# Performance work log

Measured on AMD Instinct MI355X. Metric: run time of the kernel, lower is better.

Reference implementation:

```python
import jax, jax.numpy as jnp
import numpy as np

K = 20
EPS = 1e-5
NEG_SLOPE = 0.2


def _bn(x, gamma, beta, axes):
    # batch-norm in training mode (batch statistics), per-channel on last axis
    mean = jnp.mean(x, axis=axes, keepdims=True)
    var = jnp.var(x, axis=axes, keepdims=True)
    return gamma * (x - mean) * jax.lax.rsqrt(var + EPS) + beta


def _lrelu(x):
    return jnp.where(x >= 0, x, NEG_SLOPE * x)


def setup_inputs() -> dict:
    key = jax.random.key(0)
    ks = jax.random.split(key, 8)
    B, C, N = 8, 6, 4096

    def w(k_, shape):
        fan_in = shape[-1]
        return jax.random.normal(k_, shape, jnp.float32) / np.sqrt(fan_in)

    return {
        "x": jax.random.normal(ks[0], (B, C, N), jnp.float32),
        "conv1_w": w(ks[1], (64, 12)),
        "bn1_g": jnp.ones((64,), jnp.float32), "bn1_b": jnp.zeros((64,), jnp.float32),
        "conv2_w": w(ks[2], (128, 64)),
        "bn2_g": jnp.ones((128,), jnp.float32), "bn2_b": jnp.zeros((128,), jnp.float32),
        "conv3_w": w(ks[3], (1024, 128)),
        "bn3_g": jnp.ones((1024,), jnp.float32), "bn3_b": jnp.zeros((1024,), jnp.float32),
        "fc1_w": w(ks[4], (512, 1024)),
        "bn4_g": jnp.ones((512,), jnp.float32), "bn4_b": jnp.zeros((512,), jnp.float32),
        "fc2_w": w(ks[5], (256, 512)),
        "bn5_g": jnp.ones((256,), jnp.float32), "bn5_b": jnp.zeros((256,), jnp.float32),
        "fc3_w": w(ks[6], (9, 256)), "fc3_b": jnp.zeros((9,), jnp.float32),
        "fc4_w": w(ks[7], (3, 256)), "fc4_b": jnp.zeros((3,), jnp.float32),
    }


def _get_graph_feature(x, k):
    # x: [B, C, N] -> [B, N, k, 2C]
    B, C, N = x.shape
    xt = jnp.transpose(x, (0, 2, 1))                      # [B, N, C]
    xx = jnp.sum(xt * xt, axis=-1)                        # [B, N]
    inner = jnp.einsum('bnc,bmc->bnm', xt, xt)            # [B, N, N]
    pd = 2.0 * inner - xx[:, :, None] - xx[:, None, :]    # -||xi-xj||^2
    _, idx = jax.lax.top_k(pd, k)                         # [B, N, k]
    nbr = xt[jnp.arange(B)[:, None, None], idx]           # [B, N, k, C]
    center = jnp.broadcast_to(xt[:, :, None, :], nbr.shape)
    return jnp.concatenate([nbr - center, center], axis=-1)  # [B, N, k, 2C]


def reference(x, conv1_w, bn1_g, bn1_b, conv2_w, bn2_g, bn2_b,
              conv3_w, bn3_g, bn3_b, fc1_w, bn4_g, bn4_b,
              fc2_w, bn5_g, bn5_b, fc3_w, fc3_b, fc4_w, fc4_b):
    B = x.shape[0]
    feat = _get_graph_feature(x, K)                            # [B, N, k, 12]
    h = _lrelu(_bn(jnp.einsum('bnkc,oc->bnko', feat, conv1_w), bn1_g, bn1_b, (0, 1, 2)))
    h = _lrelu(_bn(jnp.einsum('bnkc,oc->bnko', h, conv2_w), bn2_g, bn2_b, (0, 1, 2)))
    h = jnp.max(h, axis=2)                                     # [B, N, 128] max over k
    h = _lrelu(_bn(jnp.einsum('bnc,oc->bno', h, conv3_w), bn3_g, bn3_b, (0, 1)))
    g = jnp.max(h, axis=1)                                     # [B, 1024] max over points
    g = _lrelu(_bn(g @ fc1_w.T, bn4_g, bn4_b, (0,)))           # [B, 512]
    g = _lrelu(_bn(g @ fc2_w.T, bn5_g, bn5_b, (0,)))           # [B, 256]
    bias = (g @ fc4_w.T + fc4_b)[:, None, :]                   # [B, 1, 3]
    matrix = jnp.eye(3, dtype=x.dtype) + (g @ fc3_w.T + fc3_b).reshape(B, 3, 3)
    xyz = jnp.transpose(x[:, :3, :], (0, 2, 1))                # [B, N, 3]
    out = jnp.einsum('bnc,bcd->bnd', xyz, matrix) + bias       # [B, N, 3]
    return jnp.transpose(out, (0, 2, 1))                       # [B, 3, N]
```

## Files before the change

kernel.cpp:

```cpp
#include <hip/hip_runtime.h>
#include <math.h>
#include <stddef.h>


static constexpr float EPS_ = 1e-5f;

__global__ __launch_bounds__(256) void k_prep(const float* __restrict__ x,
                                              float* __restrict__ xtp)
{
    int i = blockIdx.x*256 + threadIdx.x;
    int b = i >> 12, n = i & 4095;
    const float* xb = x + (size_t)b*6*4096 + n;
    float v0 = xb[0], v1 = xb[4096], v2 = xb[2*4096];
    float v3 = xb[3*4096], v4 = xb[4*4096], v5 = xb[5*4096];
    float xx = v0*v0 + v1*v1 + v2*v2 + v3*v3 + v4*v4 + v5*v5;
    float4* o = (float4*)(xtp + (size_t)i*8);
    o[0] = make_float4(v0, v1, v2, v3);
    o[1] = make_float4(v4, v5, xx, 0.f);
}

__device__ __forceinline__ float pd_calc(const float4 a0, const float4 a1,
                                         const float4 q0, const float4 q1)
{
    float dot = a0.x*q0.x;
    dot = fmaf(a0.y, q0.y, dot);
    dot = fmaf(a0.z, q0.z, dot);
    dot = fmaf(a0.w, q0.w, dot);
    dot = fmaf(a1.x, q1.x, dot);
    dot = fmaf(a1.y, q1.y, dot);
    return fmaf(2.f, dot, -a1.z - q1.z);
}

#define TK_CAP 384
__global__ __launch_bounds__(256) void k_topk(const float* __restrict__ xtp,
                                              int* __restrict__ idxout)
{
    __shared__ float maxs[4][256];
    __shared__ float candv[4][TK_CAP];
    __shared__ int   candi[4][TK_CAP];
    __shared__ float Ts[4];
    __shared__ unsigned ccnt[4];

    const int t = threadIdx.x;
    const int rowbase = blockIdx.x << 2;
    const int b = rowbase >> 12;
    const float* xb = xtp + ((size_t)b << 15);

    float4 c0[4], c1[4];
    #pragma unroll
    for (int c = 0; c < 4; c++){
        const float4* p = (const float4*)(xtp + (size_t)(rowbase + c)*8);
        c0[c] = p[0]; c1[c] = p[1];
    }

    float mx[4] = {-INFINITY, -INFINITY, -INFINITY, -INFINITY};
    for (int i = 0; i < 16; i++){
        const float4* p = (const float4*)(xb + (size_t)((i << 8) | t)*8);
        float4 q0 = p[0], q1 = p[1];
        #pragma unroll
        for (int c = 0; c < 4; c++)
            mx[c] = fmaxf(mx[c], pd_calc(c0[c], c1[c], q0, q1));
    }
    #pragma unroll
    for (int c = 0; c < 4; c++) maxs[c][t] = mx[c];
    if (t < 4) ccnt[t] = 0u;
    __syncthreads();

    const int w = t >> 6, lane = t & 63;
    {
        float v[4];
        #pragma unroll
        for (int j = 0; j < 4; j++) v[j] = maxs[w][(j << 6) | lane];
        float gv = -INFINITY;
        for (int r = 0; r < 20; r++){
            float bv = fmaxf(fmaxf(v[0], v[1]), fmaxf(v[2], v[3]));
            gv = bv;
            #pragma unroll
            for (int s = 1; s < 64; s <<= 1) gv = fmaxf(gv, __shfl_xor(gv, s));
            if (bv == gv){
                if      (v[0] == gv) v[0] = -INFINITY;
                else if (v[1] == gv) v[1] = -INFINITY;
                else if (v[2] == gv) v[2] = -INFINITY;
                else                 v[3] = -INFINITY;
            }
        }
        if (lane == 0) Ts[w] = gv;
    }
    __syncthreads();

    #pragma unroll
    for (int c = 0; c < 4; c++){
        if (mx[c] >= Ts[c]){
            float Tc = Ts[c];
            for (int i = 0; i < 16; i++){
                int m = (i << 8) | t;
                const float4* p = (const float4*)(xb + (size_t)m*8);
                float4 q0 = p[0], q1 = p[1];
                float pd = pd_calc(c0[c], c1[c], q0, q1);
                if (pd >= Tc){
                    unsigned pos = atomicAdd(&ccnt[c], 1u);
                    if (pos < TK_CAP){ candv[c][pos] = pd; candi[c][pos] = m; }
                }
            }
        }
    }
    __syncthreads();

    {
        int n = (int)min(ccnt[w], (unsigned)TK_CAP);
        float v[6]; int id[6];
        #pragma unroll
        for (int j = 0; j < 6; j++){
            int p = (j << 6) | lane;
            bool ok = p < n;
            v[j]  = ok ? candv[w][p] : -INFINITY;
            id[j] = ok ? candi[w][p] : 0x7fffffff;
        }
        int* out = idxout + (size_t)(rowbase + w)*20;
        for (int r = 0; r < 20; r++){
            float bv = -INFINITY; int bi = 0x7fffffff, bj = 0;
            #pragma unroll
            for (int j = 0; j < 6; j++){
                bool better = (v[j] > bv) || (v[j] == bv && id[j] < bi);
                if (better){ bv = v[j]; bi = id[j]; bj = j; }
            }
            float gv = bv; int gi = bi;
            #pragma unroll
            for (int s = 1; s < 64; s <<= 1){
                float ov = __shfl_xor(gv, s); int oi = __shfl_xor(gi, s);
                if (ov > gv || (ov == gv && oi < gi)){ gv = ov; gi = oi; }
            }
            if (lane == 0) out[r] = (gi == 0x7fffffff) ? 0 : gi;
            if (bi == gi){ v[bj] = -INFINITY; id[bj] = 0x7fffffff; }
        }
    }
}

__global__ __launch_bounds__(256) void k_bn1stats(const float* __restrict__ xtp,
                                                  const int* __restrict__ idxb,
                                                  const float* __restrict__ w1,
                                                  float* __restrict__ bn1sum,
                                                  float* __restrict__ bn1sq)
{
    __shared__ float fT[320*12];
    __shared__ float red[2][4][64];
    const int t = threadIdx.x;
    const int rowbase = blockIdx.x << 4;
    const int b = rowbase >> 12;

    for (int s = t; s < 320; s += 256){
        int r = s / 20, k = s % 20;
        int grow = rowbase + r;
        int m = idxb[(size_t)grow*20 + k];
        const float4* pn = (const float4*)(xtp + (size_t)((b << 12) | m)*8);
        const float4* pc = (const float4*)(xtp + (size_t)grow*8);
        float4 n0 = pn[0], n1 = pn[1], c0 = pc[0], c1 = pc[1];
        float* f = fT + s*12;
        ((float4*)f)[0] = make_float4(n0.x-c0.x, n0.y-c0.y, n0.z-c0.z, n0.w-c0.w);
        ((float4*)f)[1] = make_float4(n1.x-c1.x, n1.y-c1.y, c0.x, c0.y);
        ((float4*)f)[2] = make_float4(c0.z, c0.w, c1.x, c1.y);
    }
    __syncthreads();
    const int o = t & 63, grp = t >> 6;
    float w[12];
    #pragma unroll
    for (int c = 0; c < 12; c++) w[c] = w1[o*12 + c];
    float sm = 0.f, sq = 0.f;
    for (int s = grp*80; s < grp*80 + 80; s++){
        const float* f = fT + s*12;
        float4 f0 = *(const float4*)(f);
        float4 fa = *(const float4*)(f + 4);
        float4 fb = *(const float4*)(f + 8);
        float h = w[0]*f0.x + w[1]*f0.y + w[2]*f0.z + w[3]*f0.w
                + w[4]*fa.x + w[5]*fa.y + w[6]*fa.z + w[7]*fa.w
                + w[8]*fb.x + w[9]*fb.y + w[10]*fb.z + w[11]*fb.w;
        sm += h; sq = fmaf(h, h, sq);
    }
    red[0][grp][o] = sm; red[1][grp][o] = sq;
    __syncthreads();
    if (t < 64){
        float a = red[0][0][t] + red[0][1][t] + red[0][2][t] + red[0][3][t];
        float c2 = red[1][0][t] + red[1][1][t] + red[1][2][t] + red[1][3][t];
        atomicAdd(bn1sum + t, a);
        atomicAdd(bn1sq + t, c2);
    }
}

__global__ void k_bnfin(const float* __restrict__ sum, const float* __restrict__ sq,
                        const float* __restrict__ gamma, const float* __restrict__ beta,
                        float* __restrict__ st, int C, float invN)
{
    int o = threadIdx.x;
    if (o < C){
        float mean = sum[o]*invN;
        float var  = sq[o]*invN - mean*mean;
        float s = gamma[o]/sqrtf(var + EPS_);
        st[o] = s;
        st[C + o] = beta[o] - mean*s;
    }
}

__global__ __launch_bounds__(256) void k_conv12(
    const float* __restrict__ xtp, const int* __restrict__ idxb,
    const float* __restrict__ w1, const float* __restrict__ w2,
    const float* __restrict__ bn1st,
    float* __restrict__ h2max, float* __restrict__ bn2sum, float* __restrict__ bn2sq)
{
    __shared__ float fT[4*20*12];
    __shared__ float f1s[4*20*64];
    __shared__ float w2t[64*132];
    __shared__ float w1s[64*13];
    const int t = threadIdx.x;
    const int rowbase = blockIdx.x << 2;
    const int b = rowbase >> 12;

    for (int e = t; e < 64*12; e += 256) w1s[(e/12)*13 + (e%12)] = w1[e];
    for (int e = t; e < 128*64; e += 256) w2t[(e & 63)*132 + (e >> 6)] = w2[e];
    if (t < 80){
        int r = t / 20, k = t % 20;
        int grow = rowbase + r;
        int m = idxb[(size_t)grow*20 + k];
        const float4* pn = (const float4*)(xtp + (size_t)((b << 12) | m)*8);
        const float4* pc = (const float4*)(xtp + (size_t)grow*8);
        float4 n0 = pn[0], n1 = pn[1], c0 = pc[0], c1 = pc[1];
        float* f = fT + (r*20 + k)*12;
        ((float4*)f)[0] = make_float4(n0.x-c0.x, n0.y-c0.y, n0.z-c0.z, n0.w-c0.w);
        ((float4*)f)[1] = make_float4(n1.x-c1.x, n1.y-c1.y, c0.x, c0.y);
        ((float4*)f)[2] = make_float4(c0.z, c0.w, c1.x, c1.y);
    }
    __syncthreads();
    {
        const int j = t & 63;
        const float s1 = bn1st[j], t1 = bn1st[64 + j];
        float wr[12];
        #pragma unroll
        for (int c = 0; c < 12; c++) wr[c] = w1s[j*13 + c];
        for (int vid = t; vid < 4*20*64; vid += 256){
            const float* f = fT + (vid >> 6)*12;
            float4 f0 = *(const float4*)(f);
            float4 fa = *(const float4*)(f + 4);
            float4 fb = *(const float4*)(f + 8);
            float acc = wr[0]*f0.x + wr[1]*f0.y + wr[2]*f0.z + wr[3]*f0.w
                      + wr[4]*fa.x + wr[5]*fa.y + wr[6]*fa.z + wr[7]*fa.w
                      + wr[8]*fb.x + wr[9]*fb.y + wr[10]*fb.z + wr[11]*fb.w;
            float v = fmaf(s1, acc, t1);
            f1s[vid] = fmaxf(v, 0.2f*v);
        }
    }
    __syncthreads();
    const int oq = t & 31, kslot = t >> 5;
    const int o0 = oq << 2;
    float mx[4][4], sm[4][4], sq[4][4];
    #pragma unroll
    for (int r = 0; r < 4; r++)
        #pragma unroll
        for (int i = 0; i < 4; i++){ mx[r][i] = -INFINITY; sm[r][i] = 0.f; sq[r][i] = 0.f; }
    for (int k = kslot; k < 20; k += 8){
        float h[4][4];
        #pragma unroll
        for (int r = 0; r < 4; r++){ h[r][0]=0.f; h[r][1]=0.f; h[r][2]=0.f; h[r][3]=0.f; }
        for (int j = 0; j < 64; j += 4){
            float wv[4][4];
            #pragma unroll
            for (int jj = 0; jj < 4; jj++)
                *(float4*)wv[jj] = *(const float4*)&w2t[(j + jj)*132 + o0];
            #pragma unroll
            for (int r = 0; r < 4; r++){
                float fv[4];
                *(float4*)fv = *(const float4*)&f1s[((r*20 + k) << 6) + j];
                #pragma unroll
                for (int jj = 0; jj < 4; jj++)
                    #pragma unroll
                    for (int oi = 0; oi < 4; oi++)
                        h[r][oi] = fmaf(fv[jj], wv[jj][oi], h[r][oi]);
            }
        }
        #pragma unroll
        for (int r = 0; r < 4; r++)
            #pragma unroll
            for (int oi = 0; oi < 4; oi++){
                mx[r][oi] = fmaxf(mx[r][oi], h[r][oi]);
                sm[r][oi] += h[r][oi];
                sq[r][oi] = fmaf(h[r][oi], h[r][oi], sq[r][oi]);
            }
    }
    __syncthreads();
    #pragma unroll
    for (int r = 0; r < 4; r++)
        *(float4*)&f1s[((kslot << 2) + r)*128 + o0] = make_float4(mx[r][0], mx[r][1], mx[r][2], mx[r][3]);
    __syncthreads();
    for (int it = t; it < 512; it += 256){
        int r = it >> 7, o = it & 127;
        float m = f1s[r*128 + o];
        #pragma unroll
        for (int ks = 1; ks < 8; ks++) m = fmaxf(m, f1s[((ks << 2) + r)*128 + o]);
        h2max[(size_t)(rowbase + r)*128 + o] = m;
    }
    __syncthreads();
    #pragma unroll
    for (int r = 0; r < 4; r++)
        *(float4*)&f1s[((kslot << 2) + r)*128 + o0] = make_float4(sm[r][0], sm[r][1], sm[r][2], sm[r][3]);
    __syncthreads();
    if (t < 128){
        float s = 0.f;
        #pragma unroll
        for (int i = 0; i < 32; i++) s += f1s[i*128 + t];
        atomicAdd(bn2sum + t, s);
    }
    __syncthreads();
    #pragma unroll
    for (int r = 0; r < 4; r++)
        *(float4*)&f1s[((kslot << 2) + r)*128 + o0] = make_float4(sq[r][0], sq[r][1], sq[r][2], sq[r][3]);
    __syncthreads();
    if (t < 128){
        float s = 0.f;
        #pragma unroll
        for (int i = 0; i < 32; i++) s += f1s[i*128 + t];
        atomicAdd(bn2sq + t, s);
    }
}

__global__ __launch_bounds__(256) void k_conv3(const float* __restrict__ h2max,
    const float* __restrict__ bn2st, const float* __restrict__ w3,
    float* __restrict__ bn3sum, float* __restrict__ bn3sq, unsigned int* __restrict__ gkey)
{
    __shared__ float f2[32*132];
    __shared__ float w3t[128*68];
    const int t = threadIdx.x;
    const int rt = blockIdx.x >> 4;
    const int ot = blockIdx.x & 15;
    const int rowbase = rt << 5;
    const int obase = ot << 6;
    const int b = rowbase >> 12;

    for (int e = t; e < 32*128; e += 256){
        int r = e >> 7, c = e & 127;
        float v = h2max[(size_t)(rowbase + r)*128 + c];
        float u = fmaf(bn2st[c], v, bn2st[128 + c]);
        f2[r*132 + c] = fmaxf(u, 0.2f*u);
    }
    for (int e = t; e < 64*128; e += 256){
        int ol = e >> 7, j = e & 127;
        w3t[j*68 + ol] = w3[(size_t)(obase + ol)*128 + j];
    }
    __syncthreads();
    const int oq = t & 15, rg = t >> 4;
    const int o0 = oq << 2, r0 = rg << 1;
    float h0[4] = {0.f,0.f,0.f,0.f}, h1[4] = {0.f,0.f,0.f,0.f};
    for (int j = 0; j < 128; j += 4){
        float wv[4][4];
        #pragma unroll
        for (int jj = 0; jj < 4; jj++)
            *(float4*)wv[jj] = *(const float4*)&w3t[(j + jj)*68 + o0];
        float fa[4], fb[4];
        *(float4*)fa = *(const float4*)&f2[r0*132 + j];
        *(float4*)fb = *(const float4*)&f2[(r0 + 1)*132 + j];
        #pragma unroll
        for (int jj = 0; jj < 4; jj++)
            #pragma unroll
            for (int oi = 0; oi < 4; oi++){
                h0[oi] = fmaf(fa[jj], wv[jj][oi], h0[oi]);
                h1[oi] = fmaf(fb[jj], wv[jj][oi], h1[oi]);
            }
    }
    __syncthreads();
    float* scratch = f2;
    *(float4*)&scratch[(rg << 6) + o0] =
        make_float4(h0[0]+h1[0], h0[1]+h1[1], h0[2]+h1[2], h0[3]+h1[3]);
    __syncthreads();
    if (t < 64){
        float s = 0.f;
        #pragma unroll
        for (int g2 = 0; g2 < 16; g2++) s += scratch[(g2 << 6) + t];
        atomicAdd(bn3sum + obase + t, s);
    }
    __syncthreads();
    *(float4*)&scratch[(rg << 6) + o0] =
        make_float4(h0[0]*h0[0]+h1[0]*h1[0], h0[1]*h0[1]+h1[1]*h1[1],
                    h0[2]*h0[2]+h1[2]*h1[2], h0[3]*h0[3]+h1[3]*h1[3]);
    __syncthreads();
    if (t < 64){
        float s = 0.f;
        #pragma unroll
        for (int g2 = 0; g2 < 16; g2++) s += scratch[(g2 << 6) + t];
        atomicAdd(bn3sq + obase + t, s);
    }
    __syncthreads();
    *(float4*)&scratch[(rg << 6) + o0] =
        make_float4(fmaxf(h0[0],h1[0]), fmaxf(h0[1],h1[1]),
                    fmaxf(h0[2],h1[2]), fmaxf(h0[3],h1[3]));
    __syncthreads();
    if (t < 64){
        float m = scratch[t];
        #pragma unroll
        for (int g2 = 1; g2 < 16; g2++) m = fmaxf(m, scratch[(g2 << 6) + t]);
        unsigned u = __float_as_uint(m);
        unsigned key = (u & 0x80000000u) ? ~u : (u | 0x80000000u);
        atomicMax(gkey + (b << 10) + obase + t, key);
    }
}

__global__ void k_bn3g(const float* __restrict__ sum, const float* __restrict__ sq,
                       const unsigned int* __restrict__ gkey,
                       const float* __restrict__ gamma, const float* __restrict__ beta,
                       float* __restrict__ g)
{
    int o = blockIdx.x*256 + threadIdx.x;
    if (o < 1024){
        float mean = sum[o]*(1.f/32768.f);
        float var  = sq[o]*(1.f/32768.f) - mean*mean;
        float s = gamma[o]/sqrtf(var + EPS_);
        float tt = beta[o] - mean*s;
        for (int b = 0; b < 8; b++){
            unsigned k = gkey[(b << 10) + o];
            unsigned u = (k & 0x80000000u) ? (k & 0x7fffffffu) : ~k;
            float v = __uint_as_float(u);
            float xv = fmaf(s, v, tt);
            g[(b << 10) + o] = fmaxf(xv, 0.2f*xv);
        }
    }
}

__global__ __launch_bounds__(256) void k_fc(const float* __restrict__ in,
                                            const float* __restrict__ w,
                                            float* __restrict__ out, int Kdim, int Odim)
{
    int wid = (blockIdx.x*256 + threadIdx.x) >> 6;
    int lane = threadIdx.x & 63;
    int nout = 8*Odim;
    if (wid >= nout) return;
    int b = wid / Odim, o = wid - b*Odim;
    const float* gi = in + (size_t)b*Kdim;
    const float* wr = w + (size_t)o*Kdim;
    float acc = 0.f;
    for (int c = lane; c < Kdim; c += 64) acc = fmaf(gi[c], wr[c], acc);
    #pragma unroll
    for (int s = 32; s > 0; s >>= 1) acc += __shfl_xor(acc, s);
    if (lane == 0) out[(size_t)b*Odim + o] = acc;
}

__global__ void k_bnb(const float* __restrict__ h, const float* __restrict__ gamma,
                      const float* __restrict__ beta, float* __restrict__ g, int C)
{
    int o = blockIdx.x*256 + threadIdx.x;
    if (o < C){
        float s = 0.f, q = 0.f;
        for (int b = 0; b < 8; b++){ float v = h[(size_t)b*C + o]; s += v; q = fmaf(v, v, q); }
        float mean = s*0.125f;
        float var  = q*0.125f - mean*mean;
        float sc = gamma[o]/sqrtf(var + EPS_);
        float tt = beta[o] - mean*sc;
        for (int b = 0; b < 8; b++){
            float xv = fmaf(sc, h[(size_t)b*C + o], tt);
            g[(size_t)b*C + o] = fmaxf(xv, 0.2f*xv);
        }
    }
}

__global__ void k_head(const float* __restrict__ g5,
                       const float* __restrict__ fc3w, const float* __restrict__ fc3b,
                       const float* __restrict__ fc4w, const float* __restrict__ fc4b,
                       float* __restrict__ mat, float* __restrict__ bias3)
{
    int t = threadIdx.x;
    if (t < 96){
        int b = t / 12, j = t % 12;
        const float* gi = g5 + b*256;
        if (j < 9){
            const float* w = fc3w + j*256;
            float a = fc3b[j];
            for (int c = 0; c < 256; c++) a = fmaf(gi[c], w[c], a);
            if (j == 0 || j == 4 || j == 8) a += 1.f;
            mat[b*9 + j] = a;
        } else {
            int d = j - 9;
            const float* w = fc4w + d*256;
            float a = fc4b[d];
            for (int c = 0; c < 256; c++) a = fmaf(gi[c], w[c], a);
            bias3[b*3 + d] = a;
        }
    }
}

__global__ __launch_bounds__(256) void k_out(const float* __restrict__ x,
                                             const float* __restrict__ mat,
                                             const float* __restrict__ bias3,
                                             float* __restrict__ out)
{
    int i = blockIdx.x*256 + threadIdx.x;
    int n = i & 4095, bd = i >> 12;
    int b = bd / 3, d = bd - b*3;
    const float* xb = x + (size_t)b*6*4096 + n;
    const float* M = mat + b*9;
    out[i] = xb[0]*M[d] + xb[4096]*M[3 + d] + xb[2*4096]*M[6 + d] + bias3[b*3 + d];
}

extern "C" void kernel_launch(void* const* d_in, const int* in_sizes, int n_in,
                              void* d_out, int out_size, void* d_ws, size_t ws_size,
                              hipStream_t stream)
{
    const float* x     = (const float*)d_in[0];
    const float* w1    = (const float*)d_in[1];
    const float* bn1g  = (const float*)d_in[2];
    const float* bn1b  = (const float*)d_in[3];
    const float* w2    = (const float*)d_in[4];
    const float* bn2g  = (const float*)d_in[5];
    const float* bn2b  = (const float*)d_in[6];
    const float* w3    = (const float*)d_in[7];
    const float* bn3gm = (const float*)d_in[8];
    const float* bn3bt = (const float*)d_in[9];
    const float* fc1w  = (const float*)d_in[10];
    const float* bn4g  = (const float*)d_in[11];
    const float* bn4b  = (const float*)d_in[12];
    const float* fc2w  = (const float*)d_in[13];
    const float* bn5g  = (const float*)d_in[14];
    const float* bn5b  = (const float*)d_in[15];
    const float* fc3w  = (const float*)d_in[16];
    const float* fc3b  = (const float*)d_in[17];
    const float* fc4w  = (const float*)d_in[18];
    const float* fc4b  = (const float*)d_in[19];
    float* out = (float*)d_out;

    char* ws = (char*)d_ws;
    float* xtp   = (float*)(ws);
    int*   idxb  = (int*)  (ws + 1048576);
    float* h2max = (float*)(ws + 3670016);
    float* zs    = (float*)(ws + 20447232);
    float* bn1sum = zs;            float* bn1sq = zs + 64;
    float* bn2sum = zs + 128;      float* bn2sq = zs + 256;
    float* bn3sum = zs + 384;      float* bn3sq = zs + 1408;
    unsigned int* gkey = (unsigned int*)(zs + 2432);
    float* tail  = (float*)(ws + 20489728);
    float* bn1st = tail;
    float* bn2st = tail + 128;
    float* g     = tail + 384;
    float* h4    = tail + 8576;
    float* g4    = tail + 12672;
    float* h5    = tail + 16768;
    float* g5    = tail + 18816;
    float* mat   = tail + 20864;
    float* bias3 = tail + 20936;

    hipMemsetAsync(zs, 0, 42496, stream);

    k_prep    <<<128,   256, 0, stream>>>(x, xtp);
    k_topk    <<<8192,  256, 0, stream>>>(xtp, idxb);
    k_bn1stats<<<2048,  256, 0, stream>>>(xtp, idxb, w1, bn1sum, bn1sq);
    k_bnfin   <<<1,     128, 0, stream>>>(bn1sum, bn1sq, bn1g, bn1b, bn1st, 64, 1.f/655360.f);
    k_conv12  <<<8192,  256, 0, stream>>>(xtp, idxb, w1, w2, bn1st, h2max, bn2sum, bn2sq);
    k_bnfin   <<<1,     128, 0, stream>>>(bn2sum, bn2sq, bn2g, bn2b, bn2st, 128, 1.f/655360.f);
    k_conv3   <<<16384, 256, 0, stream>>>(h2max, bn2st, w3, bn3sum, bn3sq, gkey);
    k_bn3g    <<<4,     256, 0, stream>>>(bn3sum, bn3sq, gkey, bn3gm, bn3bt, g);
    k_fc      <<<1024,  256, 0, stream>>>(g, fc1w, h4, 1024, 512);
    k_bnb     <<<2,     256, 0, stream>>>(h4, bn4g, bn4b, g4, 512);
    k_fc      <<<512,   256, 0, stream>>>(g4, fc2w, h5, 512, 256);
    k_bnb     <<<1,     256, 0, stream>>>(h5, bn5g, bn5b, g5, 256);
    k_head    <<<1,     128, 0, stream>>>(g5, fc3w, fc3b, fc4w, fc4b, mat, bias3);
    k_out     <<<384,   256, 0, stream>>>(x, mat, bias3, out);
}
```

Before: 808.0 us.

## Split conv12 output channels across two blocks and swizzle the feature tile in LDS

Each k_conv12 block now computes only 64 of the 128 conv2 output channels, and the grid is doubled. This shrinks the staged w2 tile and drops the separate w1 copy from shared memory, so more blocks can be resident per CU; launch bounds request 4 blocks. The conv1 feature tile in LDS gets an XOR swizzle to avoid bank conflicts on the float4 reads. The cost is that every conv1 activation is computed twice, the gather is repeated per half, and the 16 k-slots spread over 20 neighbours leave the per-thread work uneven.

```diff
diff --git a/kernel.cpp b/kernel.cpp
--- a/kernel.cpp
+++ b/kernel.cpp
@@ -200,22 +200,24 @@
     }
 }
 
-__global__ __launch_bounds__(256) void k_conv12(
+__global__ __launch_bounds__(256, 4) void k_conv12(
     const float* __restrict__ xtp, const int* __restrict__ idxb,
     const float* __restrict__ w1, const float* __restrict__ w2,
     const float* __restrict__ bn1st,
     float* __restrict__ h2max, float* __restrict__ bn2sum, float* __restrict__ bn2sq)
 {
-    __shared__ float fT[4*20*12];
-    __shared__ float f1s[4*20*64];
-    __shared__ float w2t[64*132];
-    __shared__ float w1s[64*13];
+    __shared__ float fT[80*12];
+    __shared__ float f1s[80*64];
+    __shared__ float w2t[64*65];
     const int t = threadIdx.x;
-    const int rowbase = blockIdx.x << 2;
+    const int rowbase = (blockIdx.x >> 1) << 2;
+    const int obase   = (blockIdx.x & 1) << 6;
     const int b = rowbase >> 12;
 
-    for (int e = t; e < 64*12; e += 256) w1s[(e/12)*13 + (e%12)] = w1[e];
-    for (int e = t; e < 128*64; e += 256) w2t[(e & 63)*132 + (e >> 6)] = w2[e];
+    for (int e = t; e < 64*64; e += 256){
+        int ol = e >> 6, j = e & 63;
+        w2t[j*65 + ol] = w2[(size_t)(obase + ol)*64 + j];
+    }
     if (t < 80){
         int r = t / 20, k = t % 20;
         int grow = rowbase + r;
@@ -223,7 +225,7 @@
         const float4* pn = (const float4*)(xtp + (size_t)((b << 12) | m)*8);
         const float4* pc = (const float4*)(xtp + (size_t)grow*8);
         float4 n0 = pn[0], n1 = pn[1], c0 = pc[0], c1 = pc[1];
-        float* f = fT + (r*20 + k)*12;
+        float* f = fT + t*12;
         ((float4*)f)[0] = make_float4(n0.x-c0.x, n0.y-c0.y, n0.z-c0.z, n0.w-c0.w);
         ((float4*)f)[1] = make_float4(n1.x-c1.x, n1.y-c1.y, c0.x, c0.y);
         ((float4*)f)[2] = make_float4(c0.z, c0.w, c1.x, c1.y);
@@ -234,9 +236,11 @@
         const float s1 = bn1st[j], t1 = bn1st[64 + j];
         float wr[12];
         #pragma unroll
-        for (int c = 0; c < 12; c++) wr[c] = w1s[j*13 + c];
-        for (int vid = t; vid < 4*20*64; vid += 256){
-            const float* f = fT + (vid >> 6)*12;
+        for (int cc = 0; cc < 12; cc++) wr[cc] = w1[j*12 + cc];
+        const int sw_off = (((j >> 2) ) << 2) | (j & 3);
+        for (int vid = t; vid < 80*64; vid += 256){
+            int p = vid >> 6;
+            const float* f = fT + p*12;
             float4 f0 = *(const float4*)(f);
             float4 fa = *(const float4*)(f + 4);
             float4 fb = *(const float4*)(f + 8);
@@ -244,18 +248,20 @@
                       + wr[4]*fa.x + wr[5]*fa.y + wr[6]*fa.z + wr[7]*fa.w
                       + wr[8]*fb.x + wr[9]*fb.y + wr[10]*fb.z + wr[11]*fb.w;
             float v = fmaf(s1, acc, t1);
-            f1s[vid] = fmaxf(v, 0.2f*v);
-        }
-    }
-    __syncthreads();
-    const int oq = t & 31, kslot = t >> 5;
+            v = fmaxf(v, 0.2f*v);
+            f1s[(p << 6) + (((((j >> 2) ^ (p & 3))) << 2) | (j & 3))] = v;
+        }
+        (void)sw_off;
+    }
+    __syncthreads();
+    const int oq = t & 15, ks = t >> 4;
     const int o0 = oq << 2;
     float mx[4][4], sm[4][4], sq[4][4];
     #pragma unroll
     for (int r = 0; r < 4; r++)
         #pragma unroll
         for (int i = 0; i < 4; i++){ mx[r][i] = -INFINITY; sm[r][i] = 0.f; sq[r][i] = 0.f; }
-    for (int k = kslot; k < 20; k += 8){
+    for (int k = ks; k < 20; k += 16){
         float h[4][4];
         #pragma unroll
         for (int r = 0; r < 4; r++){ h[r][0]=0.f; h[r][1]=0.f; h[r][2]=0.f; h[r][3]=0.f; }
@@ -263,11 +269,13 @@
             float wv[4][4];
             #pragma unroll
             for (int jj = 0; jj < 4; jj++)
-                *(float4*)wv[jj] = *(const float4*)&w2t[(j + jj)*132 + o0];
+                *(float4*)wv[jj] = *(const float4*)&w2t[(j + jj)*65 + o0];
+            const int jc = j >> 2;
             #pragma unroll
             for (int r = 0; r < 4; r++){
+                int row = r*20 + k;
                 float fv[4];
-                *(float4*)fv = *(const float4*)&f1s[((r*20 + k) << 6) + j];
+                *(float4*)fv = *(const float4*)&f1s[(row << 6) + ((jc ^ (row & 3)) << 2)];
                 #pragma unroll
                 for (int jj = 0; jj < 4; jj++)
                     #pragma unroll
@@ -287,36 +295,36 @@
     __syncthreads();
     #pragma unroll
     for (int r = 0; r < 4; r++)
-        *(float4*)&f1s[((kslot << 2) + r)*128 + o0] = make_float4(mx[r][0], mx[r][1], mx[r][2], mx[r][3]);
-    __syncthreads();
-    for (int it = t; it < 512; it += 256){
-        int r = it >> 7, o = it & 127;
-        float m = f1s[r*128 + o];
-        #pragma unroll
-        for (int ks = 1; ks < 8; ks++) m = fmaxf(m, f1s[((ks << 2) + r)*128 + o]);
-        h2max[(size_t)(rowbase + r)*128 + o] = m;
+        *(float4*)&f1s[((ks << 2) + r)*64 + o0] = make_float4(mx[r][0], mx[r][1], mx[r][2], mx[r][3]);
+    __syncthreads();
+    if (t < 256){
+        int r = t >> 6, o = t & 63;
+        float m = f1s[r*64 + o];
+        #pragma unroll
+        for (int kk = 1; kk < 16; kk++) m = fmaxf(m, f1s[((kk << 2) + r)*64 + o]);
+        h2max[(size_t)(rowbase + r)*128 + obase + o] = m;
     }
     __syncthreads();
     #pragma unroll
     for (int r = 0; r < 4; r++)
-        *(float4*)&f1s[((kslot << 2) + r)*128 + o0] = make_float4(sm[r][0], sm[r][1], sm[r][2], sm[r][3]);
-    __syncthreads();
-    if (t < 128){
+        *(float4*)&f1s[((ks << 2) + r)*64 + o0] = make_float4(sm[r][0], sm[r][1], sm[r][2], sm[r][3]);
+    __syncthreads();
+    if (t < 64){
         float s = 0.f;
         #pragma unroll
-        for (int i = 0; i < 32; i++) s += f1s[i*128 + t];
-        atomicAdd(bn2sum + t, s);
+        for (int i = 0; i < 64; i++) s += f1s[i*64 + t];
+        atomicAdd(bn2sum + obase + t, s);
     }
     __syncthreads();
     #pragma unroll
     for (int r = 0; r < 4; r++)
-        *(float4*)&f1s[((kslot << 2) + r)*128 + o0] = make_float4(sq[r][0], sq[r][1], sq[r][2], sq[r][3]);
-    __syncthreads();
-    if (t < 128){
+        *(float4*)&f1s[((ks << 2) + r)*64 + o0] = make_float4(sq[r][0], sq[r][1], sq[r][2], sq[r][3]);
+    __syncthreads();
+    if (t < 64){
         float s = 0.f;
         #pragma unroll
-        for (int i = 0; i < 32; i++) s += f1s[i*128 + t];
-        atomicAdd(bn2sq + t, s);
+        for (int i = 0; i < 64; i++) s += f1s[i*64 + t];
+        atomicAdd(bn2sq + obase + t, s);
     }
 }
 
@@ -547,7 +555,7 @@
     k_topk    <<<8192,  256, 0, stream>>>(xtp, idxb);
     k_bn1stats<<<2048,  256, 0, stream>>>(xtp, idxb, w1, bn1sum, bn1sq);
     k_bnfin   <<<1,     128, 0, stream>>>(bn1sum, bn1sq, bn1g, bn1b, bn1st, 64, 1.f/655360.f);
-    k_conv12  <<<8192,  256, 0, stream>>>(xtp, idxb, w1, w2, bn1st, h2max, bn2sum, bn2sq);
+    k_conv12  <<<16384, 256, 0, stream>>>(xtp, idxb, w1, w2, bn1st, h2max, bn2sum, bn2sq);
     k_bnfin   <<<1,     128, 0, stream>>>(bn2sum, bn2sq, bn2g, bn2b, bn2st, 128, 1.f/655360.f);
     k_conv3   <<<16384, 256, 0, stream>>>(h2max, bn2st, w3, bn3sum, bn3sq, gkey);
     k_bn3g    <<<4,     256, 0, stream>>>(bn3sum, bn3sq, gkey, bn3gm, bn3bt, g);
```

Measured after the change: 871.3 us. +7.8%, slower.
